# Kernel optimization log

Measured on AMD Instinct MI355X. Metric: run time of the kernel, lower is better.

## Reference

```python
import jax, jax.numpy as jnp
import numpy as np

B = 4096  # number of graphs (segments)
H = 256   # hidden_aff = hidden_comp = hidden_prot
NEG = -1e30

def leaky(x):
    return jax.nn.leaky_relu(x, 0.1)

def _lin(key, fin, fout):
    k1, k2 = jax.random.split(key)
    lim = 1.0 / np.sqrt(fin)
    W = jax.random.uniform(k1, (fin, fout), jnp.float32, -lim, lim)
    b = jax.random.uniform(k2, (fout,), jnp.float32, -lim, lim)
    return W, b

def setup_inputs() -> dict:
    key = jax.random.key(0)
    ks = jax.random.split(key, 16)
    N = 262144
    comp_feature = jax.random.normal(ks[0], (N, H), jnp.float32)
    prot_feature = jax.random.normal(ks[1], (N, H), jnp.float32)
    batch_comp = jnp.sort(jax.random.randint(ks[2], (N,), 0, B, jnp.int32))
    batch_prot = jnp.sort(jax.random.randint(ks[3], (N,), 0, B, jnp.int32))
    c_aff_W, c_aff_b = _lin(ks[4], H, H)
    c_sup_W, c_sup_b = _lin(ks[5], H, H)
    p_aff_W, p_aff_b = _lin(ks[6], H, H)
    raw_W1, raw_b1 = _lin(ks[7], 3 * H, H)
    raw_W2, raw_b2 = _lin(ks[8], H, H)
    alpha_W1, alpha_b1 = _lin(ks[9], 3 * H, H)
    alpha_W2, alpha_b2 = _lin(ks[10], H, 1)
    out_W1, out_b1 = _lin(ks[11], H, H)
    out_W2, out_b2 = _lin(ks[12], H, 1)
    return dict(comp_feature=comp_feature, prot_feature=prot_feature,
                batch_comp=batch_comp, batch_prot=batch_prot,
                c_aff_W=c_aff_W, c_aff_b=c_aff_b, c_sup_W=c_sup_W, c_sup_b=c_sup_b,
                p_aff_W=p_aff_W, p_aff_b=p_aff_b,
                raw_W1=raw_W1, raw_b1=raw_b1, raw_W2=raw_W2, raw_b2=raw_b2,
                alpha_W1=alpha_W1, alpha_b1=alpha_b1, alpha_W2=alpha_W2, alpha_b2=alpha_b2,
                out_W1=out_W1, out_b1=out_b1, out_W2=out_W2, out_b2=out_b2)

def reference(comp_feature, prot_feature, batch_comp, batch_prot,
              c_aff_W, c_aff_b, c_sup_W, c_sup_b, p_aff_W, p_aff_b,
              raw_W1, raw_b1, raw_W2, raw_b2,
              alpha_W1, alpha_b1, alpha_W2, alpha_b2,
              out_W1, out_b1, out_W2, out_b2):
    comp_emb = leaky(comp_feature @ c_aff_W + c_aff_b)           # [N, H]
    prot_emb = leaky(prot_feature @ p_aff_W + p_aff_b)           # [N, H]
    prot_pool = jax.ops.segment_max(prot_emb, batch_prot, num_segments=B)  # [B, H]
    supe = jax.ops.segment_sum(leaky(comp_feature @ c_sup_W + c_sup_b),
                               batch_comp, num_segments=B)       # [B, H]
    feat = jnp.concatenate([comp_emb, supe[batch_comp], prot_pool[batch_comp]], axis=1)  # [N, 3H]
    raw = leaky(feat @ raw_W1 + raw_b1) @ raw_W2 + raw_b2        # [N, H]
    prealpha = leaky(feat @ alpha_W1 + alpha_b1) @ alpha_W2 + alpha_b2  # [N, 1]
    # scatter softmax over graphs
    seg_max = jax.ops.segment_max(prealpha, batch_comp, num_segments=B)
    a_exp = jnp.exp(prealpha - seg_max[batch_comp])
    a_sum = jax.ops.segment_sum(a_exp, batch_comp, num_segments=B) + 1e-6
    alpha = a_exp / a_sum[batch_comp]                            # [N, 1]
    vector = jax.ops.segment_sum(raw * alpha, batch_comp, num_segments=B)  # [B, H]
    affinity_pred = leaky(vector @ out_W1 + out_b1) @ out_W2 + out_b2      # [B, 1]
    return vector, alpha, affinity_pred
```

## Files before the change

### kernel.cpp

```cpp
#include <hip/hip_runtime.h>
#include <cstddef>
#include <cstdint>

#define HDIM 256
#define BSEG 4096

typedef __bf16 bf16x8 __attribute__((ext_vector_type(8)));
typedef float f32x4 __attribute__((ext_vector_type(4)));

__device__ __forceinline__ float leaky(float x) { return x >= 0.f ? x : 0.1f * x; }
__device__ __forceinline__ float bf2f(ushort u) {
    return __builtin_bit_cast(float, (uint32_t)u << 16);
}
__device__ __forceinline__ ushort f2bf(float f) {
    uint32_t x = __builtin_bit_cast(uint32_t, f);
    return (ushort)((x + 0x7fffu + ((x >> 16) & 1u)) >> 16);
}
__device__ __forceinline__ bf16x8 pack8(float4 a, float4 b) {
    union { ushort s[8]; bf16x8 v; } u;
    u.s[0] = f2bf(a.x); u.s[1] = f2bf(a.y); u.s[2] = f2bf(a.z); u.s[3] = f2bf(a.w);
    u.s[4] = f2bf(b.x); u.s[5] = f2bf(b.y); u.s[6] = f2bf(b.z); u.s[7] = f2bf(b.w);
    return u.v;
}
__device__ __forceinline__ void store_bf4(ushort* p, float v0, float v1, float v2, float v3) {
    ushort4 o; o.x = f2bf(v0); o.y = f2bf(v1); o.z = f2bf(v2); o.w = f2bf(v3);
    *(ushort4*)p = o;
}

__device__ __forceinline__ void gld16(const ushort* g, ushort* lds) {
    __builtin_amdgcn_global_load_lds(
        (const __attribute__((address_space(1))) uint32_t*)g,
        (__attribute__((address_space(3))) uint32_t*)lds, 16, 0, 0);
}

__global__ void seg_bounds_k(const int* __restrict__ bc, const int* __restrict__ bp,
                             int* __restrict__ sc, int* __restrict__ sp, int n, int nb)
{
    int t = blockIdx.x * blockDim.x + threadIdx.x;
    if (t >= 2 * (nb + 1)) return;
    bool isc = (t <= nb);
    const int* a = isc ? bc : bp;
    int v = isc ? t : t - (nb + 1);
    int lo = 0, hi = n;
    while (lo < hi) { int mid = (lo + hi) >> 1; if (a[mid] < v) lo = mid + 1; else hi = mid; }
    if (isc) sc[t] = lo; else sp[t - (nb + 1)] = lo;
}

__global__ __launch_bounds__(256) void wt_cast_all(
    const float* __restrict__ s0, const float* __restrict__ s1,
    const float* __restrict__ s2, const float* __restrict__ s3,
    const float* __restrict__ s4,
    ushort* __restrict__ d0, ushort* __restrict__ d1, ushort* __restrict__ d2,
    ushort* __restrict__ d3, ushort* __restrict__ d4)
{
    int m = blockIdx.x >> 4, tile = blockIdx.x & 15;
    const float* s = m == 0 ? s0 : m == 1 ? s1 : m == 2 ? s2 : m == 3 ? s3 : s4;
    ushort*      d = m == 0 ? d0 : m == 1 ? d1 : m == 2 ? d2 : m == 3 ? d3 : d4;
    int r0 = (tile >> 2) * 64, c0 = (tile & 3) * 64;
    __shared__ ushort t[64][72];
    int cc = threadIdx.x & 63, rr = threadIdx.x >> 6;
    for (int r = rr; r < 64; r += 4) t[cc][r] = f2bf(s[(size_t)(r0 + r) * 256 + c0 + cc]);
    __syncthreads();
    for (int r = rr; r < 64; r += 4) d[(size_t)(c0 + r) * 256 + r0 + cc] = t[r][cc];
}

__device__ __forceinline__ void tile_mma(const ushort* As, const ushort* __restrict__ WT,
        int colT, int lr, int lt, f32x4 acc[4][4])
{
    #pragma unroll
    for (int ks = 0; ks < 8; ++ks) {
        bf16x8 af[4], bv[4];
        #pragma unroll
        for (int m = 0; m < 4; ++m) {
            const int r = m * 16 + lr;
            const int c = ks * 4 + lt;
            af[m] = *(const bf16x8*)&As[(r * 32 + (c ^ (r & 7))) * 8];
        }
        #pragma unroll
        for (int n = 0; n < 4; ++n)
            bv[n] = *(const bf16x8*)&WT[(size_t)(colT + n * 16 + lr) * HDIM + ks * 32 + lt * 8];
        #pragma unroll
        for (int m = 0; m < 4; ++m)
            #pragma unroll
            for (int n = 0; n < 4; ++n)
                acc[m][n] = __builtin_amdgcn_mfma_f32_16x16x32_bf16(bv[n], af[m], acc[m][n], 0, 0, 0);
    }
}

template<int MODE>
__global__ __launch_bounds__(256, 4) void mgs(
    const float* __restrict__ Ac, const float* __restrict__ Ap,
    const ushort* __restrict__ Ahb,
    const ushort* __restrict__ WT,
    const float* __restrict__ b0, const float* __restrict__ b1, const float* __restrict__ b2,
    const float* __restrict__ rt0, const float* __restrict__ rt1,
    const int* __restrict__ idx,
    ushort* __restrict__ o0, ushort* __restrict__ o1, ushort* __restrict__ o2,
    const float* __restrict__ w2, float* __restrict__ pre, int NB)
{
    __shared__ __attribute__((aligned(16))) ushort As[64 * 256];
    __shared__ float pb[64][4];

    const int tid = threadIdx.x;
    const int l = tid & 63, w = tid >> 6;
    const int lr = l & 15, lt = l >> 4;

    const int bid = blockIdx.x;
    const bool isProt = (MODE == 0) && (bid >= NB);
    const int row0 = (isProt ? bid - NB : bid) * 64;

    if (MODE == 0) {
        const float* A = isProt ? Ap : Ac;
        #pragma unroll
        for (int i = 0; i < 8; ++i) {
            const int s = i * 256 + tid;
            const int r = s >> 5, q = s & 31;
            const float* src = A + (size_t)(row0 + r) * HDIM + ((q ^ (r & 7)) << 3);
            float4 x = *(const float4*)src;
            float4 y = *(const float4*)(src + 4);
            *(bf16x8*)&As[s * 8] = pack8(x, y);
        }
    } else {
        #pragma unroll
        for (int i = 0; i < 8; ++i) {
            const int s = i * 256 + tid;
            const int r = s >> 5, q = s & 31;
            gld16(Ahb + (size_t)(row0 + r) * HDIM + ((q ^ (r & 7)) << 3), &As[s * 8]);
        }
    }
    __syncthreads();

    if (MODE == 0) {
        const int ntile = isProt ? 1 : 2;
        #pragma unroll
        for (int t = 0; t < 2; ++t) {
            if (t >= ntile) break;
            const int colT = isProt ? (512 + w * 64) : (w * 128 + t * 64);
            f32x4 acc[4][4] = {};
            tile_mma(As, WT, colT, lr, lt, acc);
            const int g = colT >> 8;
            const float* bias = g == 0 ? b0 : g == 1 ? b1 : b2;
            ushort* outp      = g == 0 ? o0 : g == 1 ? o1 : o2;
            const int cin = (colT & 255) + (lt << 2);
            #pragma unroll
            for (int m = 0; m < 4; ++m) {
                const int row = row0 + m * 16 + lr;
                #pragma unroll
                for (int n = 0; n < 4; ++n) {
                    const int c = cin + n * 16;
                    float4 b4 = *(const float4*)&bias[c];
                    float v0 = leaky(acc[m][n][0] + b4.x);
                    float v1 = leaky(acc[m][n][1] + b4.y);
                    float v2 = leaky(acc[m][n][2] + b4.z);
                    float v3 = leaky(acc[m][n][3] + b4.w);
                    store_bf4(&outp[(size_t)row * HDIM + c], v0, v1, v2, v3);
                }
            }
        }
    } else {
        {
            const int colT = w * 64;
            f32x4 acc[4][4] = {};
            tile_mma(As, WT, colT, lr, lt, acc);
            const int cin = colT + (lt << 2);
            #pragma unroll
            for (int m = 0; m < 4; ++m) {
                const int row = row0 + m * 16 + lr;
                const float* rrow = rt0 + (size_t)idx[row] * HDIM;
                #pragma unroll
                for (int n = 0; n < 4; ++n) {
                    const int c = cin + n * 16;
                    float4 r4 = *(const float4*)&rrow[c];
                    float v0 = leaky(acc[m][n][0] + r4.x);
                    float v1 = leaky(acc[m][n][1] + r4.y);
                    float v2 = leaky(acc[m][n][2] + r4.z);
                    float v3 = leaky(acc[m][n][3] + r4.w);
                    store_bf4(&o0[(size_t)row * HDIM + c], v0, v1, v2, v3);
                }
            }
        }
        {
            const int colT = 256 + w * 64;
            f32x4 acc[4][4] = {};
            tile_mma(As, WT, colT, lr, lt, acc);
            const int cin = (colT - 256) + (lt << 2);
            #pragma unroll
            for (int m = 0; m < 4; ++m) {
                const int row = row0 + m * 16 + lr;
                const float* rrow = rt1 + (size_t)idx[row] * HDIM;
                float p = 0.f;
                #pragma unroll
                for (int n = 0; n < 4; ++n) {
                    const int c = cin + n * 16;
                    float4 r4 = *(const float4*)&rrow[c];
                    float4 w4 = *(const float4*)&w2[c];
                    p += leaky(acc[m][n][0] + r4.x) * w4.x;
                    p += leaky(acc[m][n][1] + r4.y) * w4.y;
                    p += leaky(acc[m][n][2] + r4.z) * w4.z;
                    p += leaky(acc[m][n][3] + r4.w) * w4.w;
                }
                p += __shfl_xor(p, 16);
                p += __shfl_xor(p, 32);
                if (lt == 0) pb[m * 16 + lr][w] = p;
            }
        }
        __syncthreads();
        if (tid < 64) pre[row0 + tid] = pb[tid][0] + pb[tid][1] + pb[tid][2] + pb[tid][3];
    }
}

__global__ __launch_bounds__(256) void gemm64_2(
    const float* __restrict__ A, const float* __restrict__ A2,
    const float* __restrict__ Wb_r, const float* __restrict__ Wc_r, const float* __restrict__ bias_r,
    const float* __restrict__ Wb_a, const float* __restrict__ Wc_a, const float* __restrict__ bias_a,
    float* __restrict__ Cr, float* __restrict__ Ca)
{
    const int K = HDIM, NO = HDIM;
    const float* W  = blockIdx.z ? Wb_a : Wb_r;
    const float* W2 = blockIdx.z ? Wc_a : Wc_r;
    const float* bias = blockIdx.z ? bias_a : bias_r;
    float* C = blockIdx.z ? Ca : Cr;

    __shared__ float As [16][68];
    __shared__ float Bs [16][68];
    __shared__ float As2[16][68];
    __shared__ float Bs2[16][68];

    const int tid = threadIdx.x;
    const int tx = tid & 15, ty = tid >> 4;
    const int row0 = blockIdx.x * 64, col0 = blockIdx.y * 64;

    const int lr = tid >> 2;
    const int lk = (tid & 3) << 2;
    const int bk = tid >> 4;
    const int bj = (tid & 15) << 2;

    float acc[4][4] = {};

    for (int k0 = 0; k0 < K; k0 += 16) {
        float4 a4 = *(const float4*)&A[(size_t)(row0 + lr) * K + k0 + lk];
        As[lk + 0][lr] = a4.x; As[lk + 1][lr] = a4.y;
        As[lk + 2][lr] = a4.z; As[lk + 3][lr] = a4.w;
        *(float4*)&Bs[bk][bj] = *(const float4*)&W[(size_t)(k0 + bk) * NO + col0 + bj];
        float4 c4 = *(const float4*)&A2[(size_t)(row0 + lr) * K + k0 + lk];
        As2[lk + 0][lr] = c4.x; As2[lk + 1][lr] = c4.y;
        As2[lk + 2][lr] = c4.z; As2[lk + 3][lr] = c4.w;
        *(float4*)&Bs2[bk][bj] = *(const float4*)&W2[(size_t)(k0 + bk) * NO + col0 + bj];
        __syncthreads();
        #pragma unroll
        for (int kk = 0; kk < 16; ++kk) {
            float4 av = *(const float4*)&As[kk][ty << 2];
            float4 bv = *(const float4*)&Bs[kk][tx << 2];
            float a_[4] = {av.x, av.y, av.z, av.w};
            float b_[4] = {bv.x, bv.y, bv.z, bv.w};
            #pragma unroll
            for (int i = 0; i < 4; ++i)
                #pragma unroll
                for (int j = 0; j < 4; ++j)
                    acc[i][j] += a_[i] * b_[j];
            float4 av2 = *(const float4*)&As2[kk][ty << 2];
            float4 bv2 = *(const float4*)&Bs2[kk][tx << 2];
            float c_[4] = {av2.x, av2.y, av2.z, av2.w};
            float d_[4] = {bv2.x, bv2.y, bv2.z, bv2.w};
            #pragma unroll
            for (int i = 0; i < 4; ++i)
                #pragma unroll
                for (int j = 0; j < 4; ++j)
                    acc[i][j] += c_[i] * d_[j];
        }
        __syncthreads();
    }

    #pragma unroll
    for (int i = 0; i < 4; ++i) {
        int row = row0 + (ty << 2) + i;
        float vv[4];
        #pragma unroll
        for (int j = 0; j < 4; ++j) {
            int col = col0 + (tx << 2) + j;
            vv[j] = acc[i][j] + bias[col];
        }
        float4 o; o.x = vv[0]; o.y = vv[1]; o.z = vv[2]; o.w = vv[3];
        *(float4*)&C[(size_t)row * NO + col0 + (tx << 2)] = o;
    }
}

template<bool ISMAX>
__global__ __launch_bounds__(256) void seg_reduce8(const ushort* __restrict__ in,
        const int* __restrict__ starts, float* __restrict__ out)
{
    __shared__ float part[8][HDIM];
    const int b = blockIdx.x, tid = threadIdx.x;
    const int sub = tid & 31, r = tid >> 5;
    const int s = starts[b], e = starts[b + 1];
    float a[8];
    #pragma unroll
    for (int j = 0; j < 8; ++j) a[j] = ISMAX ? -INFINITY : 0.f;
    for (int i = s + r; i < e; i += 8) {
        uint4 v = *(const uint4*)&in[(size_t)i * HDIM + sub * 8];
        float f[8] = { bf2f((ushort)v.x), bf2f((ushort)(v.x >> 16)),
                       bf2f((ushort)v.y), bf2f((ushort)(v.y >> 16)),
                       bf2f((ushort)v.z), bf2f((ushort)(v.z >> 16)),
                       bf2f((ushort)v.w), bf2f((ushort)(v.w >> 16)) };
        #pragma unroll
        for (int j = 0; j < 8; ++j) a[j] = ISMAX ? fmaxf(a[j], f[j]) : (a[j] + f[j]);
    }
    #pragma unroll
    for (int j = 0; j < 8; ++j) part[r][sub * 8 + j] = a[j];
    __syncthreads();
    float res = part[0][tid];
    #pragma unroll
    for (int j = 1; j < 8; ++j) res = ISMAX ? fmaxf(res, part[j][tid]) : (res + part[j][tid]);
    out[(size_t)b * HDIM + tid] = res;
}

__global__ __launch_bounds__(64) void seg_softmax_k(const float* __restrict__ pre,
        const int* __restrict__ starts, float* __restrict__ alpha, float* __restrict__ sa)
{
    int b = blockIdx.x, lane = threadIdx.x;
    int s = starts[b], e = starts[b + 1];
    float m = -INFINITY;
    for (int i = s + lane; i < e; i += 64) m = fmaxf(m, pre[i]);
    #pragma unroll
    for (int off = 32; off; off >>= 1) m = fmaxf(m, __shfl_xor(m, off));
    float S = 0.f;
    for (int i = s + lane; i < e; i += 64) S += expf(pre[i] - m);
    #pragma unroll
    for (int off = 32; off; off >>= 1) S += __shfl_xor(S, off);
    float denom = S + 1e-6f;
    if (lane == 0) sa[b] = S / denom;
    for (int i = s + lane; i < e; i += 64) alpha[i] = expf(pre[i] - m) / denom;
}

__global__ __launch_bounds__(256) void seg_wsum8(const ushort* __restrict__ raw,
        const float* __restrict__ alpha, const int* __restrict__ starts,
        float* __restrict__ vec)
{
    __shared__ float part[8][HDIM];
    const int b = blockIdx.x, tid = threadIdx.x;
    const int sub = tid & 31, r = tid >> 5;
    const int s = starts[b], e = starts[b + 1];
    float a[8] = {};
    for (int i = s + r; i < e; i += 8) {
        float al = alpha[i];
        uint4 v = *(const uint4*)&raw[(size_t)i * HDIM + sub * 8];
        a[0] += bf2f((ushort)v.x) * al;        a[1] += bf2f((ushort)(v.x >> 16)) * al;
        a[2] += bf2f((ushort)v.y) * al;        a[3] += bf2f((ushort)(v.y >> 16)) * al;
        a[4] += bf2f((ushort)v.z) * al;        a[5] += bf2f((ushort)(v.z >> 16)) * al;
        a[6] += bf2f((ushort)v.w) * al;        a[7] += bf2f((ushort)(v.w >> 16)) * al;
    }
    #pragma unroll
    for (int j = 0; j < 8; ++j) part[r][sub * 8 + j] = a[j];
    __syncthreads();
    float res = 0.f;
    #pragma unroll
    for (int j = 0; j < 8; ++j) res += part[j][tid];
    vec[(size_t)b * HDIM + tid] = res;
}

__global__ __launch_bounds__(256) void final_k(
    const float* __restrict__ hw, const float* __restrict__ sa,
    const float* __restrict__ W2r, const float* __restrict__ rb2,
    const float* __restrict__ oW1, const float* __restrict__ ob1,
    const float* __restrict__ oW2, const float* __restrict__ ob2,
    float* __restrict__ out_vec, float* __restrict__ out_aff)
{
    __shared__ float v[HDIM];
    __shared__ float vecs[HDIM];
    __shared__ float red[4];
    int b = blockIdx.x, t = threadIdx.x;
    v[t] = hw[(size_t)b * HDIM + t];
    __syncthreads();
    float a = rb2[t] * sa[b];
    #pragma unroll 8
    for (int k = 0; k < HDIM; ++k) a += v[k] * W2r[(size_t)k * HDIM + t];
    out_vec[(size_t)b * HDIM + t] = a;
    vecs[t] = a;
    __syncthreads();
    float h = ob1[t];
    #pragma unroll 8
    for (int k = 0; k < HDIM; ++k) h += vecs[k] * oW1[(size_t)k * HDIM + t];
    h = leaky(h);
    float p = h * oW2[t];
    #pragma unroll
    for (int off = 32; off; off >>= 1) p += __shfl_down(p, off);
    int lane = t & 63, wid = t >> 6;
    if (lane == 0) red[wid] = p;
    __syncthreads();
    if (t == 0) out_aff[b] = red[0] + red[1] + red[2] + red[3] + ob2[0];
}

extern "C" void kernel_launch(void* const* d_in, const int* in_sizes, int n_in,
                              void* d_out, int out_size, void* d_ws, size_t ws_size,
                              hipStream_t stream)
{
    const int N = in_sizes[2];
    const int H = HDIM;
    const int B = BSEG;

    const float* comp   = (const float*)d_in[0];
    const float* prot   = (const float*)d_in[1];
    const int*   bc     = (const int*)d_in[2];
    const int*   bp     = (const int*)d_in[3];
    const float* c_aff_W = (const float*)d_in[4];
    const float* c_aff_b = (const float*)d_in[5];
    const float* c_sup_W = (const float*)d_in[6];
    const float* c_sup_b = (const float*)d_in[7];
    const float* p_aff_W = (const float*)d_in[8];
    const float* p_aff_b = (const float*)d_in[9];
    const float* raw_W1  = (const float*)d_in[10];
    const float* raw_b1  = (const float*)d_in[11];
    const float* raw_W2  = (const float*)d_in[12];
    const float* raw_b2  = (const float*)d_in[13];
    const float* alpha_W1 = (const float*)d_in[14];
    const float* alpha_b1 = (const float*)d_in[15];
    const float* alpha_W2 = (const float*)d_in[16];
    const float* out_W1  = (const float*)d_in[18];
    const float* out_b1  = (const float*)d_in[19];
    const float* out_W2  = (const float*)d_in[20];
    const float* out_b2  = (const float*)d_in[21];

    const size_t NBIG = (size_t)N * H;
    const size_t SSEG = (size_t)B * H;

    char* p = (char*)d_ws;
    ushort* e1 = (ushort*)p; p += NBIG * 2;
    ushort* e2 = (ushort*)p; p += NBIG * 2;
    ushort* e3 = (ushort*)p; p += NBIG * 2;
    float* supe = (float*)p;  p += SSEG * 4;
    float* pool = (float*)p;  p += SSEG * 4;
    float* gr   = (float*)p;  p += SSEG * 4;
    float* ga   = (float*)p;  p += SSEG * 4;
    float* hw   = (float*)p;  p += SSEG * 4;
    float* sa   = (float*)p;  p += (size_t)B * 4;
    float* pre  = (float*)p;  p += (size_t)N * 4;
    ushort* WT1 = (ushort*)p; p += (size_t)512 * 256 * 2;
    ushort* WTp = (ushort*)p; p += (size_t)256 * 256 * 2;
    ushort* WT2 = (ushort*)p; p += (size_t)512 * 256 * 2;
    int* sc = (int*)p; p += (size_t)(B + 1) * 4;
    int* sp = (int*)p; p += (size_t)(B + 1) * 4;
    if ((size_t)(p - (char*)d_ws) > ws_size) return;

    ushort* h1 = e3;

    float* out_vec   = (float*)d_out;
    float* out_alpha = out_vec + SSEG;
    float* out_aff   = out_alpha + N;

    dim3 blk(256);
    const int NB = N / 64;

    seg_bounds_k<<<(2 * (B + 1) + 255) / 256, blk, 0, stream>>>(bc, bp, sc, sp, N, B);
    wt_cast_all<<<5 * 16, blk, 0, stream>>>(
        c_aff_W, c_sup_W, p_aff_W, raw_W1, alpha_W1,
        WT1, WT1 + 65536, WTp, WT2, WT2 + 65536);

    mgs<0><<<2 * NB, blk, 0, stream>>>(
        comp, prot, nullptr, WT1, c_aff_b, c_sup_b, p_aff_b,
        nullptr, nullptr, nullptr, e1, e2, e3, nullptr, nullptr, NB);
    seg_reduce8<false><<<B, blk, 0, stream>>>(e2, sc, supe);
    seg_reduce8<true ><<<B, blk, 0, stream>>>(e3, sp, pool);
    gemm64_2<<<dim3(B / 64, 4, 2), blk, 0, stream>>>(supe, pool,
        raw_W1 + H * H, raw_W1 + 2 * H * H, raw_b1,
        alpha_W1 + H * H, alpha_W1 + 2 * H * H, alpha_b1, gr, ga);
    mgs<1><<<NB, blk, 0, stream>>>(
        nullptr, nullptr, e1, WT2, nullptr, nullptr, nullptr,
        gr, ga, bc, h1, nullptr, nullptr, alpha_W2, pre, NB);
    seg_softmax_k<<<B, dim3(64), 0, stream>>>(pre, sc, out_alpha, sa);
    seg_wsum8<<<B, blk, 0, stream>>>(h1, out_alpha, sc, hw);
    final_k<<<B, blk, 0, stream>>>(hw, sa, raw_W2, raw_b2,
        out_W1, out_b1, out_W2, out_b2, out_vec, out_aff);
}
```

Baseline: 749.7 us.

## Make GEMM kernels weight-stationary with LDS-resident weight tiles and streamed activations

Replaces the activation-in-LDS GEMM kernels with a weight-stationary design. Each 512-thread workgroup loads a 128-column bf16 weight slice into LDS once and streams 1024 activation rows per block from global memory straight into registers with double-buffered loads. Blocks are remapped across XCDs, and the alpha pre-score is split into two partial sums that the softmax kernel adds together. This removes repeated global weight reads and the LDS staging of activations, but each activation row is now re-read once per column block, and the LDS footprint and register pressure grow.

Measured after the change: 2.258 ms. 201% more time.

```diff
diff --git a/kernel.cpp b/kernel.cpp
--- a/kernel.cpp
+++ b/kernel.cpp
@@ -64,148 +64,131 @@
     for (int r = rr; r < 64; r += 4) d[(size_t)(c0 + r) * 256 + r0 + cc] = t[r][cc];
 }
 
-__device__ __forceinline__ void tile_mma(const ushort* As, const ushort* __restrict__ WT,
-        int colT, int lr, int lt, f32x4 acc[4][4])
-{
-    #pragma unroll
-    for (int ks = 0; ks < 8; ++ks) {
-        bf16x8 af[4], bv[4];
-        #pragma unroll
-        for (int m = 0; m < 4; ++m) {
-            const int r = m * 16 + lr;
-            const int c = ks * 4 + lt;
-            af[m] = *(const bf16x8*)&As[(r * 32 + (c ^ (r & 7))) * 8];
-        }
-        #pragma unroll
-        for (int n = 0; n < 4; ++n)
-            bv[n] = *(const bf16x8*)&WT[(size_t)(colT + n * 16 + lr) * HDIM + ks * 32 + lt * 8];
-        #pragma unroll
-        for (int m = 0; m < 4; ++m)
-            #pragma unroll
-            for (int n = 0; n < 4; ++n)
-                acc[m][n] = __builtin_amdgcn_mfma_f32_16x16x32_bf16(bv[n], af[m], acc[m][n], 0, 0, 0);
-    }
-}
-
 template<int MODE>
-__global__ __launch_bounds__(256, 4) void mgs(
+__global__ __launch_bounds__(512, 4) void mgw(
     const float* __restrict__ Ac, const float* __restrict__ Ap,
     const ushort* __restrict__ Ahb,
     const ushort* __restrict__ WT,
     const float* __restrict__ b0, const float* __restrict__ b1, const float* __restrict__ b2,
-    const float* __restrict__ rt0, const float* __restrict__ rt1,
+    const float* __restrict__ gr, const float* __restrict__ ga,
     const int* __restrict__ idx,
     ushort* __restrict__ o0, ushort* __restrict__ o1, ushort* __restrict__ o2,
-    const float* __restrict__ w2, float* __restrict__ pre, int NB)
-{
-    __shared__ __attribute__((aligned(16))) ushort As[64 * 256];
-    __shared__ float pb[64][4];
+    const float* __restrict__ w2, float* __restrict__ pre, int Ntot)
+{
+    __shared__ __attribute__((aligned(16))) ushort Wl[128 * 256];
 
     const int tid = threadIdx.x;
     const int l = tid & 63, w = tid >> 6;
     const int lr = l & 15, lt = l >> 4;
 
-    const int bid = blockIdx.x;
-    const bool isProt = (MODE == 0) && (bid >= NB);
-    const int row0 = (isProt ? bid - NB : bid) * 64;
-
-    if (MODE == 0) {
-        const float* A = isProt ? Ap : Ac;
+    const uint nwg = gridDim.x, bid = blockIdx.x;
+    const uint orig = (bid & 7) * (nwg >> 3) + (bid >> 3);
+    const int NCB = (MODE == 0) ? 6 : 4;
+    const int rb = (int)(orig / NCB), cb = (int)(orig % NCB);
+
+    {
+        const size_t wbase = (size_t)cb * 128 * HDIM;
         #pragma unroll
         for (int i = 0; i < 8; ++i) {
-            const int s = i * 256 + tid;
-            const int r = s >> 5, q = s & 31;
-            const float* src = A + (size_t)(row0 + r) * HDIM + ((q ^ (r & 7)) << 3);
-            float4 x = *(const float4*)src;
-            float4 y = *(const float4*)(src + 4);
-            *(bf16x8*)&As[s * 8] = pack8(x, y);
+            const int s = i * 512 + tid;
+            const int col = s >> 5, pslot = s & 31;
+            const int q = pslot ^ (col & 7);
+            gld16(WT + wbase + (size_t)col * HDIM + q * 8, &Wl[s * 8]);
         }
-    } else {
-        #pragma unroll
-        for (int i = 0; i < 8; ++i) {
-            const int s = i * 256 + tid;
-            const int r = s >> 5, q = s & 31;
-            gld16(Ahb + (size_t)(row0 + r) * HDIM + ((q ^ (r & 7)) << 3), &As[s * 8]);
-        }
-    }
-    __syncthreads();
-
-    if (MODE == 0) {
-        const int ntile = isProt ? 1 : 2;
-        #pragma unroll
-        for (int t = 0; t < 2; ++t) {
-            if (t >= ntile) break;
-            const int colT = isProt ? (512 + w * 64) : (w * 128 + t * 64);
-            f32x4 acc[4][4] = {};
-            tile_mma(As, WT, colT, lr, lt, acc);
-            const int g = colT >> 8;
-            const float* bias = g == 0 ? b0 : g == 1 ? b1 : b2;
-            ushort* outp      = g == 0 ? o0 : g == 1 ? o1 : o2;
-            const int cin = (colT & 255) + (lt << 2);
-            #pragma unroll
-            for (int m = 0; m < 4; ++m) {
-                const int row = row0 + m * 16 + lr;
+    }
+    asm volatile("s_waitcnt vmcnt(0)" ::: "memory");
+    __builtin_amdgcn_s_barrier();
+
+    const int r0w = rb * 1024 + w * 128;
+
+    #pragma unroll 1
+    for (int g = 0; g < 8; ++g) {
+        const int r0 = r0w + g * 16;
+        f32x4 acc[8] = {};
+
+        if (MODE == 0) {
+            const float* A = (cb < 4) ? Ac : Ap;
+            const float* fsrc = A + (size_t)(r0 + lr) * HDIM + lt * 8;
+            float4 ra[2][2];
+            ra[0][0] = *(const float4*)(fsrc + 0);  ra[0][1] = *(const float4*)(fsrc + 4);
+            ra[1][0] = *(const float4*)(fsrc + 32); ra[1][1] = *(const float4*)(fsrc + 36);
+            #pragma unroll
+            for (int ks = 0; ks < 8; ++ks) {
+                bf16x8 af = pack8(ra[ks & 1][0], ra[ks & 1][1]);
+                if (ks < 6) {
+                    ra[ks & 1][0] = *(const float4*)(fsrc + (ks + 2) * 32);
+                    ra[ks & 1][1] = *(const float4*)(fsrc + (ks + 2) * 32 + 4);
+                }
                 #pragma unroll
-                for (int n = 0; n < 4; ++n) {
-                    const int c = cin + n * 16;
-                    float4 b4 = *(const float4*)&bias[c];
-                    float v0 = leaky(acc[m][n][0] + b4.x);
-                    float v1 = leaky(acc[m][n][1] + b4.y);
-                    float v2 = leaky(acc[m][n][2] + b4.z);
-                    float v3 = leaky(acc[m][n][3] + b4.w);
-                    store_bf4(&outp[(size_t)row * HDIM + c], v0, v1, v2, v3);
+                for (int n = 0; n < 8; ++n) {
+                    const int col = n * 16 + lr;
+                    const int p = (ks * 4 + lt) ^ (col & 7);
+                    bf16x8 bv = *(const bf16x8*)&Wl[(col * 32 + p) * 8];
+                    acc[n] = __builtin_amdgcn_mfma_f32_16x16x32_bf16(bv, af, acc[n], 0, 0, 0);
+                }
+            }
+        } else {
+            const ushort* hsrc = Ahb + (size_t)(r0 + lr) * HDIM + lt * 8;
+            bf16x8 ra[2];
+            ra[0] = *(const bf16x8*)(hsrc + 0);
+            ra[1] = *(const bf16x8*)(hsrc + 32);
+            #pragma unroll
+            for (int ks = 0; ks < 8; ++ks) {
+                bf16x8 af = ra[ks & 1];
+                if (ks < 6) ra[ks & 1] = *(const bf16x8*)(hsrc + (ks + 2) * 32);
+                #pragma unroll
+                for (int n = 0; n < 8; ++n) {
+                    const int col = n * 16 + lr;
+                    const int p = (ks * 4 + lt) ^ (col & 7);
+                    bf16x8 bv = *(const bf16x8*)&Wl[(col * 32 + p) * 8];
+                    acc[n] = __builtin_amdgcn_mfma_f32_16x16x32_bf16(bv, af, acc[n], 0, 0, 0);
                 }
             }
         }
-    } else {
-        {
-            const int colT = w * 64;
-            f32x4 acc[4][4] = {};
-            tile_mma(As, WT, colT, lr, lt, acc);
-            const int cin = colT + (lt << 2);
-            #pragma unroll
-            for (int m = 0; m < 4; ++m) {
-                const int row = row0 + m * 16 + lr;
-                const float* rrow = rt0 + (size_t)idx[row] * HDIM;
-                #pragma unroll
-                for (int n = 0; n < 4; ++n) {
-                    const int c = cin + n * 16;
-                    float4 r4 = *(const float4*)&rrow[c];
-                    float v0 = leaky(acc[m][n][0] + r4.x);
-                    float v1 = leaky(acc[m][n][1] + r4.y);
-                    float v2 = leaky(acc[m][n][2] + r4.z);
-                    float v3 = leaky(acc[m][n][3] + r4.w);
-                    store_bf4(&o0[(size_t)row * HDIM + c], v0, v1, v2, v3);
-                }
+
+        const int row = r0 + lr;
+        if (MODE == 0) {
+            const int e = cb >> 1;
+            const float* bias = e == 0 ? b0 : e == 1 ? b1 : b2;
+            ushort* outp      = e == 0 ? o0 : e == 1 ? o1 : o2;
+            const int coloff = (cb & 1) * 128;
+            #pragma unroll
+            for (int n = 0; n < 8; ++n) {
+                const int c = coloff + n * 16 + lt * 4;
+                float4 b4 = *(const float4*)&bias[c];
+                store_bf4(&outp[(size_t)row * HDIM + c],
+                          leaky(acc[n][0] + b4.x), leaky(acc[n][1] + b4.y),
+                          leaky(acc[n][2] + b4.z), leaky(acc[n][3] + b4.w));
             }
+        } else if (cb < 2) {
+            const int coloff = cb * 128;
+            const float* rrow = gr + (size_t)idx[row] * HDIM;
+            #pragma unroll
+            for (int n = 0; n < 8; ++n) {
+                const int c = coloff + n * 16 + lt * 4;
+                float4 r4 = *(const float4*)&rrow[c];
+                store_bf4(&o0[(size_t)row * HDIM + c],
+                          leaky(acc[n][0] + r4.x), leaky(acc[n][1] + r4.y),
+                          leaky(acc[n][2] + r4.z), leaky(acc[n][3] + r4.w));
+            }
+        } else {
+            const int coloff = (cb - 2) * 128;
+            const float* rrow = ga + (size_t)idx[row] * HDIM;
+            float p = 0.f;
+            #pragma unroll
+            for (int n = 0; n < 8; ++n) {
+                const int c = coloff + n * 16 + lt * 4;
+                float4 r4 = *(const float4*)&rrow[c];
+                float4 w4 = *(const float4*)&w2[c];
+                p += leaky(acc[n][0] + r4.x) * w4.x;
+                p += leaky(acc[n][1] + r4.y) * w4.y;
+                p += leaky(acc[n][2] + r4.z) * w4.z;
+                p += leaky(acc[n][3] + r4.w) * w4.w;
+            }
+            p += __shfl_xor(p, 16);
+            p += __shfl_xor(p, 32);
+            if (lt == 0) pre[(size_t)(cb - 2) * Ntot + row] = p;
         }
-        {
-            const int colT = 256 + w * 64;
-            f32x4 acc[4][4] = {};
-            tile_mma(As, WT, colT, lr, lt, acc);
-            const int cin = (colT - 256) + (lt << 2);
-            #pragma unroll
-            for (int m = 0; m < 4; ++m) {
-                const int row = row0 + m * 16 + lr;
-                const float* rrow = rt1 + (size_t)idx[row] * HDIM;
-                float p = 0.f;
-                #pragma unroll
-                for (int n = 0; n < 4; ++n) {
-                    const int c = cin + n * 16;
-                    float4 r4 = *(const float4*)&rrow[c];
-                    float4 w4 = *(const float4*)&w2[c];
-                    p += leaky(acc[m][n][0] + r4.x) * w4.x;
-                    p += leaky(acc[m][n][1] + r4.y) * w4.y;
-                    p += leaky(acc[m][n][2] + r4.z) * w4.z;
-                    p += leaky(acc[m][n][3] + r4.w) * w4.w;
-                }
-                p += __shfl_xor(p, 16);
-                p += __shfl_xor(p, 32);
-                if (lt == 0) pb[m * 16 + lr][w] = p;
-            }
-        }
-        __syncthreads();
-        if (tid < 64) pre[row0 + tid] = pb[tid][0] + pb[tid][1] + pb[tid][2] + pb[tid][3];
     }
 }
 
@@ -314,22 +297,23 @@
     out[(size_t)b * HDIM + tid] = res;
 }
 
-__global__ __launch_bounds__(64) void seg_softmax_k(const float* __restrict__ pre,
-        const int* __restrict__ starts, float* __restrict__ alpha, float* __restrict__ sa)
+__global__ __launch_bounds__(64) void seg_softmax_k(const float* __restrict__ p0,
+        const float* __restrict__ p1, const int* __restrict__ starts,
+        float* __restrict__ alpha, float* __restrict__ sa)
 {
     int b = blockIdx.x, lane = threadIdx.x;
     int s = starts[b], e = starts[b + 1];
     float m = -INFINITY;
-    for (int i = s + lane; i < e; i += 64) m = fmaxf(m, pre[i]);
+    for (int i = s + lane; i < e; i += 64) m = fmaxf(m, p0[i] + p1[i]);
     #pragma unroll
     for (int off = 32; off; off >>= 1) m = fmaxf(m, __shfl_xor(m, off));
     float S = 0.f;
-    for (int i = s + lane; i < e; i += 64) S += expf(pre[i] - m);
+    for (int i = s + lane; i < e; i += 64) S += expf(p0[i] + p1[i] - m);
     #pragma unroll
     for (int off = 32; off; off >>= 1) S += __shfl_xor(S, off);
     float denom = S + 1e-6f;
     if (lane == 0) sa[b] = S / denom;
-    for (int i = s + lane; i < e; i += 64) alpha[i] = expf(pre[i] - m) / denom;
+    for (int i = s + lane; i < e; i += 64) alpha[i] = expf(p0[i] + p1[i] - m) / denom;
 }
 
 __global__ __launch_bounds__(256) void seg_wsum8(const ushort* __restrict__ raw,
@@ -433,13 +417,14 @@
     float* ga   = (float*)p;  p += SSEG * 4;
     float* hw   = (float*)p;  p += SSEG * 4;
     float* sa   = (float*)p;  p += (size_t)B * 4;
-    float* pre  = (float*)p;  p += (size_t)N * 4;
+    float* pre  = (float*)p;  p += (size_t)2 * N * 4;
     ushort* WT1 = (ushort*)p; p += (size_t)512 * 256 * 2;
     ushort* WTp = (ushort*)p; p += (size_t)256 * 256 * 2;
     ushort* WT2 = (ushort*)p; p += (size_t)512 * 256 * 2;
     int* sc = (int*)p; p += (size_t)(B + 1) * 4;
     int* sp = (int*)p; p += (size_t)(B + 1) * 4;
     if ((size_t)(p - (char*)d_ws) > ws_size) return;
+    (void)WTp;
 
     ushort* h1 = e3;
 
@@ -447,26 +432,25 @@
     float* out_alpha = out_vec + SSEG;
     float* out_aff   = out_alpha + N;
 
-    dim3 blk(256);
-    const int NB = N / 64;
+    dim3 blk(256), blkW(512);
 
     seg_bounds_k<<<(2 * (B + 1) + 255) / 256, blk, 0, stream>>>(bc, bp, sc, sp, N, B);
     wt_cast_all<<<5 * 16, blk, 0, stream>>>(
         c_aff_W, c_sup_W, p_aff_W, raw_W1, alpha_W1,
         WT1, WT1 + 65536, WTp, WT2, WT2 + 65536);
 
-    mgs<0><<<2 * NB, blk, 0, stream>>>(
+    mgw<0><<<6 * (N / 1024), blkW, 0, stream>>>(
         comp, prot, nullptr, WT1, c_aff_b, c_sup_b, p_aff_b,
-        nullptr, nullptr, nullptr, e1, e2, e3, nullptr, nullptr, NB);
+        nullptr, nullptr, nullptr, e1, e2, e3, nullptr, nullptr, N);
     seg_reduce8<false><<<B, blk, 0, stream>>>(e2, sc, supe);
     seg_reduce8<true ><<<B, blk, 0, stream>>>(e3, sp, pool);
     gemm64_2<<<dim3(B / 64, 4, 2), blk, 0, stream>>>(supe, pool,
         raw_W1 + H * H, raw_W1 + 2 * H * H, raw_b1,
         alpha_W1 + H * H, alpha_W1 + 2 * H * H, alpha_b1, gr, ga);
-    mgs<1><<<NB, blk, 0, stream>>>(
+    mgw<1><<<4 * (N / 1024), blkW, 0, stream>>>(
         nullptr, nullptr, e1, WT2, nullptr, nullptr, nullptr,
-        gr, ga, bc, h1, nullptr, nullptr, alpha_W2, pre, NB);
-    seg_softmax_k<<<B, dim3(64), 0, stream>>>(pre, sc, out_alpha, sa);
+        gr, ga, bc, h1, nullptr, nullptr, alpha_W2, pre, N);
+    seg_softmax_k<<<B, dim3(64), 0, stream>>>(pre, pre + N, sc, out_alpha, sa);
     seg_wsum8<<<B, blk, 0, stream>>>(h1, out_alpha, sc, hw);
     final_k<<<B, blk, 0, stream>>>(hw, sa, raw_W2, raw_b2,
         out_W1, out_b1, out_W2, out_b2, out_vec, out_aff);
```
